# Kernel optimization log

Hardware: AMD Instinct MI355X
Metric: run time of the kernel (lower is better)

The kernel has to match this reference:

```python
import math
import jax, jax.numpy as jnp
import numpy as np

SR = 44100
N_HARMONICS = 64
EPS = 1e-5
LOG10 = math.log(10.0)


def scale_function(x):
    # ddsp_pytorch util.scale_function: 2 * sigmoid(x)**log(10) + 1e-7
    return 2.0 * jax.nn.sigmoid(x) ** LOG10 + 1e-7


def setup_inputs() -> dict:
    key = jax.random.key(0)
    k1, k2, k3 = jax.random.split(key, 3)
    bs, n_samples = 32, 64000
    # f0 in [80, 480] Hz so upper harmonics cross Nyquist for some frames
    f0_hz = jax.random.uniform(k1, (bs, n_samples), dtype=jnp.float32) * 400.0 + 80.0
    harmonic_amplitudes = jax.random.normal(k2, (bs, n_samples, N_HARMONICS + 1), dtype=jnp.float32)
    phase = jax.random.uniform(k3, (bs,), dtype=jnp.float32) * 2.0 * jnp.pi
    return {"f0_hz": f0_hz, "harmonic_amplitudes": harmonic_amplitudes, "phase": phase}


def reference(f0_hz, harmonic_amplitudes, phase):
    ha = scale_function(harmonic_amplitudes)            # (bs, S, H+1)
    f0 = f0_hz[..., None]                               # (bs, S, 1)
    total_amplitude = ha[..., :1]                       # (bs, S, 1)
    ha = ha[..., 1:]                                    # (bs, S, H)
    harm = jnp.arange(1, N_HARMONICS + 1, dtype=f0.dtype)  # (H,)
    # anti-alias: zero harmonics above Nyquist
    aa = (f0 * harm < SR / 2).astype(f0.dtype)
    ha_aa = ha * aa
    ha_aa = ha_aa / (jnp.sum(ha_aa, axis=-1, keepdims=True) + EPS)
    ha_aa = ha_aa * total_amplitude
    # phase integration
    omega = jnp.cumsum(2.0 * jnp.pi * f0 / SR, axis=1)  # (bs, S, 1)
    omega = omega + phase.reshape(-1, 1, 1)
    omegas = omega * harm                               # (bs, S, H)
    signal = jnp.sum(jnp.sin(omegas) * ha_aa, axis=-1)  # (bs, S)
    return signal
```

## Files before the change

kernel.cpp:

```cpp
#include <hip/hip_runtime.h>
#include <math.h>

#define BATCH    32
#define CHUNK    128
#define NCHUNK   500
#define TAB_N    1152

__device__ __forceinline__ float scale_fn(float x) {
    float e = exp2f(-1.4426950408889634f * x);
    float l = log2f(1.0f + e);
    return 2.0f * exp2f(-2.302585092994046f * l) + 1e-7f;
}

__global__ __launch_bounds__(128) void table_kernel(float* __restrict__ gtab) {
    int i = blockIdx.x * 128 + threadIdx.x;
    if (i < TAB_N) gtab[i] = scale_fn(fmaf((float)i, 0.015625f, -8.0f));
}

__global__ __launch_bounds__(128) void chunk_sum_kernel(
        const float* __restrict__ f0, double* __restrict__ csum) {
    int bx = blockIdx.x;
    int t  = threadIdx.x;
    double v = (double)f0[(long)bx * CHUNK + t];
    for (int off = 32; off > 0; off >>= 1) v += __shfl_down(v, off, 64);
    __shared__ double ws[2];
    if ((t & 63) == 0) ws[t >> 6] = v;
    __syncthreads();
    if (t == 0) csum[bx] = ws[0] + ws[1];
}

__global__ __launch_bounds__(512) void chunk_scan_kernel(double* __restrict__ csum) {
    int r = blockIdx.x;
    int t = threadIdx.x;
    int lane = t & 63, w = t >> 6;
    double orig = (t < NCHUNK) ? csum[(long)r * NCHUNK + t] : 0.0;
    double v = orig;
    for (int off = 1; off < 64; off <<= 1) {
        double n = __shfl_up(v, off, 64);
        if (lane >= off) v += n;
    }
    __shared__ double wsum[8];
    if (lane == 63) wsum[w] = v;
    __syncthreads();
    double add = 0.0;
    for (int i = 0; i < w; ++i) add += wsum[i];
    v += add;
    if (t < NCHUNK) csum[(long)r * NCHUNK + t] = v - orig;
}

__global__ __launch_bounds__(128) void osc_kernel(
        const float* __restrict__ f0,
        const float* __restrict__ ha,
        const float* __restrict__ phase,
        const double* __restrict__ csum,
        const float* __restrict__ gtab,
        float* __restrict__ out) {
    int bx = blockIdx.x;
    int r  = bx / NCHUNK;
    int t  = threadIdx.x;
    int lane = t & 63, w = t >> 6;

    long sbase = (long)bx * CHUNK;
    const float* hablk = ha + sbase * 65;

    __shared__ float amp[CHUNK * 65];
    __shared__ float tab[TAB_N];

    {
        const float4* ts = (const float4*)gtab;
        float4* td = (float4*)tab;
        td[t]       = ts[t];
        td[t + 128] = ts[t + 128];
        if (t < 32) td[t + 256] = ts[t + 256];
    }
    {
        const float4* src = (const float4*)hablk;
        float4* dst = (float4*)amp;
        #pragma unroll
        for (int i = 0; i < 16; ++i)
            dst[i * 128 + t] = src[i * 128 + t];
        if (t < 32)
            dst[16 * 128 + t] = src[16 * 128 + t];
    }

    float f0v = f0[sbase + t];

    double v = (double)f0v;
    for (int off = 1; off < 64; off <<= 1) {
        double n = __shfl_up(v, off, 64);
        if (lane >= off) v += n;
    }
    __shared__ double wsum[2];
    if (lane == 63) wsum[w] = v;
    __syncthreads();
    if (w == 1) v += wsum[0];
    v += csum[bx];
    double x = v * (1.0 / 44100.0) + (double)phase[r] * 0.15915494309189535;
    x -= floor(x);
    float nu = (float)x;

    float k0 = floorf(22050.0f / f0v);
    if (f0v * (k0 + 1.0f) < 22050.0f)      k0 += 1.0f;
    else if (!(f0v * k0 < 22050.0f))       k0 -= 1.0f;

    float th = 6.283185307179586f * nu;
    float s1 = __sinf(th);
    float c1 = __cosf(th);
    float s = s1, c = c1;

    float S1 = 0.0f, S2 = 0.0f;
    #pragma unroll 8
    for (int h = 0; h < 64; ++h) {
        float a  = amp[t * 65 + 1 + h];
        float tc = fmaf(a, 64.0f, 512.0f);
        tc = fminf(fmaxf(tc, 0.0f), 1022.99f);
        float fi = floorf(tc);
        int   i  = (int)fi;
        float fr = tc - fi;
        float w0 = tab[i];
        float w1 = tab[i + 1];
        float wv = fmaf(fr, w1 - w0, w0);
        wv = ((float)(h + 1) <= k0) ? wv : 0.0f;
        S1 += wv;
        S2 = fmaf(wv, s, S2);
        float ns = fmaf(s, c1,  c * s1);
        float nc = fmaf(c, c1, -(s * s1));
        s = ns; c = nc;
    }

    float total = scale_fn(amp[t * 65]);
    out[sbase + t] = total * S2 / (S1 + 1e-5f);
}

extern "C" void kernel_launch(void* const* d_in, const int* in_sizes, int n_in,
                              void* d_out, int out_size, void* d_ws, size_t ws_size,
                              hipStream_t stream) {
    const float* f0    = (const float*)d_in[0];
    const float* ha    = (const float*)d_in[1];
    const float* phase = (const float*)d_in[2];
    float* out = (float*)d_out;

    double* csum = (double*)d_ws;
    float*  gtab = (float*)((char*)d_ws + 131072);

    table_kernel<<<(TAB_N + 127) / 128, 128, 0, stream>>>(gtab);
    chunk_sum_kernel<<<BATCH * NCHUNK, CHUNK, 0, stream>>>(f0, csum);
    chunk_scan_kernel<<<BATCH, 512, 0, stream>>>(csum);
    osc_kernel<<<BATCH * NCHUNK, CHUNK, 0, stream>>>(f0, ha, phase, csum, gtab, out);
}
```

Measured before the change: 703.0 us.

## Compute scaled amplitudes during load into fp16 LDS slab, drop lookup table

Replaces the precomputed lookup-table interpolation with a direct sigmoid-power evaluation done while loading from global memory. Results are stored as fp16 in a padded shared slab, with the anti-alias mask applied at that point. The inner loop then reads half2 pairs and uses a two-term Chebyshev sine recurrence. This cuts shared memory (allowing the occupancy hint of 4) and removes the per-harmonic table gathers. In exchange the transcendental work moves into the load phase, and fp16 storage (scaled by 256) costs some precision.

```diff
diff --git a/kernel.cpp b/kernel.cpp
--- a/kernel.cpp
+++ b/kernel.cpp
@@ -1,20 +1,16 @@
 #include <hip/hip_runtime.h>
+#include <hip/hip_fp16.h>
 #include <math.h>
 
-#define BATCH    32
-#define CHUNK    128
-#define NCHUNK   500
-#define TAB_N    1152
+#define BATCH      32
+#define CHUNK      128
+#define NCHUNK     500
+#define SLABSTRIDE 66
 
-__device__ __forceinline__ float scale_fn(float x) {
+__device__ __forceinline__ float scale256(float x) {
     float e = exp2f(-1.4426950408889634f * x);
     float l = log2f(1.0f + e);
-    return 2.0f * exp2f(-2.302585092994046f * l) + 1e-7f;
-}
-
-__global__ __launch_bounds__(128) void table_kernel(float* __restrict__ gtab) {
-    int i = blockIdx.x * 128 + threadIdx.x;
-    if (i < TAB_N) gtab[i] = scale_fn(fmaf((float)i, 0.015625f, -8.0f));
+    return fmaf(512.0f, exp2f(-2.302585092994046f * l), 256.0f * 1e-7f);
 }
 
 __global__ __launch_bounds__(128) void chunk_sum_kernel(
@@ -48,12 +44,30 @@
     if (t < NCHUNK) csum[(long)r * NCHUNK + t] = v - orig;
 }
 
-__global__ __launch_bounds__(128) void osc_kernel(
+__device__ __forceinline__ void process4(float4 v, int e,
+        __half* __restrict__ slab, float* __restrict__ amp0,
+        const float* __restrict__ f0s) {
+    int s = e / 65;
+    int c = e - s * 65;
+    float vals[4] = {v.x, v.y, v.z, v.w};
+    #pragma unroll
+    for (int k = 0; k < 4; ++k) {
+        float wv = scale256(vals[k]);
+        if (c == 0) {
+            amp0[s] = wv * 0.00390625f;
+        } else {
+            bool keep = f0s[s] * (float)c < 22050.0f;
+            slab[s * SLABSTRIDE + (c - 1)] = __float2half(keep ? wv : 0.0f);
+        }
+        if (++c == 65) { c = 0; ++s; }
+    }
+}
+
+__global__ __launch_bounds__(128, 4) void osc_kernel(
         const float* __restrict__ f0,
         const float* __restrict__ ha,
         const float* __restrict__ phase,
         const double* __restrict__ csum,
-        const float* __restrict__ gtab,
         float* __restrict__ out) {
     int bx = blockIdx.x;
     int r  = bx / NCHUNK;
@@ -61,36 +75,32 @@
     int lane = t & 63, w = t >> 6;
 
     long sbase = (long)bx * CHUNK;
-    const float* hablk = ha + sbase * 65;
 
-    __shared__ float amp[CHUNK * 65];
-    __shared__ float tab[TAB_N];
+    __shared__ __half slab[CHUNK * SLABSTRIDE];
+    __shared__ float  amp0[CHUNK];
+    __shared__ float  f0s[CHUNK];
+    __shared__ double wsum[2];
 
-    {
-        const float4* ts = (const float4*)gtab;
-        float4* td = (float4*)tab;
-        td[t]       = ts[t];
-        td[t + 128] = ts[t + 128];
-        if (t < 32) td[t + 256] = ts[t + 256];
+    if (t < 32) ((float4*)f0s)[t] = ((const float4*)(f0 + sbase))[t];
+    __syncthreads();
+
+    const float4* src = (const float4*)(ha + sbase * 65);
+    #pragma unroll 4
+    for (int i = 0; i < 16; ++i) {
+        float4 v = src[i * 128 + t];
+        process4(v, (i * 128 + t) * 4, slab, amp0, f0s);
     }
-    {
-        const float4* src = (const float4*)hablk;
-        float4* dst = (float4*)amp;
-        #pragma unroll
-        for (int i = 0; i < 16; ++i)
-            dst[i * 128 + t] = src[i * 128 + t];
-        if (t < 32)
-            dst[16 * 128 + t] = src[16 * 128 + t];
+    if (t < 32) {
+        float4 v = src[2048 + t];
+        process4(v, (2048 + t) * 4, slab, amp0, f0s);
     }
 
-    float f0v = f0[sbase + t];
-
+    float f0v = f0s[t];
     double v = (double)f0v;
     for (int off = 1; off < 64; off <<= 1) {
         double n = __shfl_up(v, off, 64);
         if (lane >= off) v += n;
     }
-    __shared__ double wsum[2];
     if (lane == 63) wsum[w] = v;
     __syncthreads();
     if (w == 1) v += wsum[0];
@@ -99,52 +109,38 @@
     x -= floor(x);
     float nu = (float)x;
 
-    float k0 = floorf(22050.0f / f0v);
-    if (f0v * (k0 + 1.0f) < 22050.0f)      k0 += 1.0f;
-    else if (!(f0v * k0 < 22050.0f))       k0 -= 1.0f;
-
     float th = 6.283185307179586f * nu;
-    float s1 = __sinf(th);
-    float c1 = __cosf(th);
-    float s = s1, c = c1;
+    float sA = __sinf(th);
+    float c2 = 2.0f * __cosf(th);
+    float sB = c2 * sA;
 
     float S1 = 0.0f, S2 = 0.0f;
-    #pragma unroll 8
-    for (int h = 0; h < 64; ++h) {
-        float a  = amp[t * 65 + 1 + h];
-        float tc = fmaf(a, 64.0f, 512.0f);
-        tc = fminf(fmaxf(tc, 0.0f), 1022.99f);
-        float fi = floorf(tc);
-        int   i  = (int)fi;
-        float fr = tc - fi;
-        float w0 = tab[i];
-        float w1 = tab[i + 1];
-        float wv = fmaf(fr, w1 - w0, w0);
-        wv = ((float)(h + 1) <= k0) ? wv : 0.0f;
-        S1 += wv;
-        S2 = fmaf(wv, s, S2);
-        float ns = fmaf(s, c1,  c * s1);
-        float nc = fmaf(c, c1, -(s * s1));
-        s = ns; c = nc;
+    const __half2* row = (const __half2*)(slab + t * SLABSTRIDE);
+    #pragma unroll
+    for (int j = 0; j < 32; ++j) {
+        float2 w2 = __half22float2(row[j]);
+        S1 += w2.x; S2 = fmaf(w2.x, sA, S2);
+        S1 += w2.y; S2 = fmaf(w2.y, sB, S2);
+        float sn1 = fmaf(c2, sB, -sA);
+        float sn2 = fmaf(c2, sn1, -sB);
+        sA = sn1; sB = sn2;
     }
 
-    float total = scale_fn(amp[t * 65]);
-    out[sbase + t] = total * S2 / (S1 + 1e-5f);
+    out[sbase + t] = amp0[t] * S2 / (S1 + 256.0f * 1e-5f);
 }
 
 extern "C" void kernel_launch(void* const* d_in, const int* in_sizes, int n_in,
                               void* d_out, int out_size, void* d_ws, size_t ws_size,
                               hipStream_t stream) {
+    (void)in_sizes; (void)n_in; (void)out_size; (void)ws_size;
     const float* f0    = (const float*)d_in[0];
     const float* ha    = (const float*)d_in[1];
     const float* phase = (const float*)d_in[2];
     float* out = (float*)d_out;
 
     double* csum = (double*)d_ws;
-    float*  gtab = (float*)((char*)d_ws + 131072);
 
-    table_kernel<<<(TAB_N + 127) / 128, 128, 0, stream>>>(gtab);
     chunk_sum_kernel<<<BATCH * NCHUNK, CHUNK, 0, stream>>>(f0, csum);
     chunk_scan_kernel<<<BATCH, 512, 0, stream>>>(csum);
-    osc_kernel<<<BATCH * NCHUNK, CHUNK, 0, stream>>>(f0, ha, phase, csum, gtab, out);
+    osc_kernel<<<BATCH * NCHUNK, CHUNK, 0, stream>>>(f0, ha, phase, csum, out);
 }
```

After: 749.8 us. +6.7%, slower.

## Split harmonics across four lanes per sample with 512-thread oscillator blocks

Applied to the files above, without the earlier changes.

The oscillator kernel now launches 512 threads per 128-sample chunk, and each sample's 64 harmonics are divided among 4 lanes of 16 harmonics each. Partial sums are combined with cross-lane shuffles. The harmonic sine recurrence is replaced by a Chebyshev two-term recurrence seeded per lane from directly computed sines, and the phase scan runs on only the first 128 threads via shared memory. The aim is more threads in flight to hide global and LDS latency, and shorter serial dependency chains per thread, at the cost of extra barriers and shuffles and fewer resident blocks per CU given the shared-memory footprint.

```diff
diff --git a/kernel.cpp b/kernel.cpp
--- a/kernel.cpp
+++ b/kernel.cpp
@@ -48,7 +48,7 @@
     if (t < NCHUNK) csum[(long)r * NCHUNK + t] = v - orig;
 }
 
-__global__ __launch_bounds__(128) void osc_kernel(
+__global__ __launch_bounds__(512, 4) void osc_kernel(
         const float* __restrict__ f0,
         const float* __restrict__ ha,
         const float* __restrict__ phase,
@@ -63,78 +63,106 @@
     long sbase = (long)bx * CHUNK;
     const float* hablk = ha + sbase * 65;
 
-    __shared__ float amp[CHUNK * 65];
-    __shared__ float tab[TAB_N];
+    __shared__ float  amp[CHUNK * 65];
+    __shared__ float  tab[TAB_N];
+    __shared__ float  f0s[CHUNK];
+    __shared__ float  nuA[CHUNK];
+    __shared__ double wsum[2];
 
-    {
-        const float4* ts = (const float4*)gtab;
-        float4* td = (float4*)tab;
-        td[t]       = ts[t];
-        td[t + 128] = ts[t + 128];
-        if (t < 32) td[t + 256] = ts[t + 256];
-    }
+    if (t < 288) ((float4*)tab)[t] = ((const float4*)gtab)[t];
+    if (t < 32)  ((float4*)f0s)[t] = ((const float4*)(f0 + sbase))[t];
     {
         const float4* src = (const float4*)hablk;
         float4* dst = (float4*)amp;
         #pragma unroll
-        for (int i = 0; i < 16; ++i)
-            dst[i * 128 + t] = src[i * 128 + t];
-        if (t < 32)
-            dst[16 * 128 + t] = src[16 * 128 + t];
+        for (int i = 0; i < 4; ++i)
+            dst[i * 512 + t] = src[i * 512 + t];
+        if (t < 32) dst[2048 + t] = src[2048 + t];
     }
+    __syncthreads();
 
-    float f0v = f0[sbase + t];
+    double v = 0.0;
+    if (t < 128) {
+        v = (double)f0s[t];
+        for (int off = 1; off < 64; off <<= 1) {
+            double n = __shfl_up(v, off, 64);
+            if (lane >= off) v += n;
+        }
+        if (lane == 63) wsum[w] = v;
+    }
+    __syncthreads();
+    if (t < 128) {
+        if (w == 1) v += wsum[0];
+        v += csum[bx];
+        double x = v * (1.0 / 44100.0) + (double)phase[r] * 0.15915494309189535;
+        x -= floor(x);
+        nuA[t] = (float)x;
+    }
+    __syncthreads();
 
-    double v = (double)f0v;
-    for (int off = 1; off < 64; off <<= 1) {
-        double n = __shfl_up(v, off, 64);
-        if (lane >= off) v += n;
-    }
-    __shared__ double wsum[2];
-    if (lane == 63) wsum[w] = v;
-    __syncthreads();
-    if (w == 1) v += wsum[0];
-    v += csum[bx];
-    double x = v * (1.0 / 44100.0) + (double)phase[r] * 0.15915494309189535;
-    x -= floor(x);
-    float nu = (float)x;
+    int s  = w * 16 + (lane & 15);
+    int q  = lane >> 4;
+    int h0 = q * 16;
+
+    float f0v = f0s[s];
+    float nu  = nuA[s];
 
     float k0 = floorf(22050.0f / f0v);
     if (f0v * (k0 + 1.0f) < 22050.0f)      k0 += 1.0f;
     else if (!(f0v * k0 < 22050.0f))       k0 -= 1.0f;
 
-    float th = 6.283185307179586f * nu;
-    float s1 = __sinf(th);
-    float c1 = __cosf(th);
-    float s = s1, c = c1;
+    float c2;
+    {
+        float th = 6.283185307179586f * nu;
+        c2 = 2.0f * __cosf(th);
+    }
+    float m1 = (float)(h0 + 1) * nu; m1 -= floorf(m1);
+    float m2 = (float)(h0 + 2) * nu; m2 -= floorf(m2);
+    float sA = __sinf(6.283185307179586f * m1);
+    float sB = 6.283185307179586f * m2;  sB = __sinf(sB);
+
+    const float* arow = amp + s * 65 + 1 + h0;
 
     float S1 = 0.0f, S2 = 0.0f;
-    #pragma unroll 8
-    for (int h = 0; h < 64; ++h) {
-        float a  = amp[t * 65 + 1 + h];
-        float tc = fmaf(a, 64.0f, 512.0f);
-        tc = fminf(fmaxf(tc, 0.0f), 1022.99f);
-        float fi = floorf(tc);
-        int   i  = (int)fi;
-        float fr = tc - fi;
-        float w0 = tab[i];
-        float w1 = tab[i + 1];
-        float wv = fmaf(fr, w1 - w0, w0);
-        wv = ((float)(h + 1) <= k0) ? wv : 0.0f;
-        S1 += wv;
-        S2 = fmaf(wv, s, S2);
-        float ns = fmaf(s, c1,  c * s1);
-        float nc = fmaf(c, c1, -(s * s1));
-        s = ns; c = nc;
+    #pragma unroll
+    for (int j = 0; j < 16; j += 2) {
+        float a0 = arow[j];
+        float a1 = arow[j + 1];
+        float tc0 = fmaf(a0, 64.0f, 512.0f);
+        tc0 = fminf(fmaxf(tc0, 0.0f), 1022.99f);
+        float fi0 = floorf(tc0); int i0 = (int)fi0; float fr0 = tc0 - fi0;
+        float w0 = fmaf(fr0, tab[i0 + 1] - tab[i0], tab[i0]);
+        float tc1 = fmaf(a1, 64.0f, 512.0f);
+        tc1 = fminf(fmaxf(tc1, 0.0f), 1022.99f);
+        float fi1 = floorf(tc1); int i1 = (int)fi1; float fr1 = tc1 - fi1;
+        float w1 = fmaf(fr1, tab[i1 + 1] - tab[i1], tab[i1]);
+
+        w0 = ((float)(h0 + 1 + j) <= k0) ? w0 : 0.0f;
+        w1 = ((float)(h0 + 2 + j) <= k0) ? w1 : 0.0f;
+
+        S1 += w0; S2 = fmaf(w0, sA, S2);
+        S1 += w1; S2 = fmaf(w1, sB, S2);
+
+        float sn1 = fmaf(c2, sB, -sA);
+        float sn2 = fmaf(c2, sn1, -sB);
+        sA = sn1; sB = sn2;
     }
 
-    float total = scale_fn(amp[t * 65]);
-    out[sbase + t] = total * S2 / (S1 + 1e-5f);
+    S1 += __shfl_xor(S1, 16, 64);
+    S1 += __shfl_xor(S1, 32, 64);
+    S2 += __shfl_xor(S2, 16, 64);
+    S2 += __shfl_xor(S2, 32, 64);
+
+    if (q == 0) {
+        float total = scale_fn(amp[s * 65]);
+        out[sbase + s] = total * S2 / (S1 + 1e-5f);
+    }
 }
 
 extern "C" void kernel_launch(void* const* d_in, const int* in_sizes, int n_in,
                               void* d_out, int out_size, void* d_ws, size_t ws_size,
                               hipStream_t stream) {
+    (void)in_sizes; (void)n_in; (void)out_size; (void)ws_size;
     const float* f0    = (const float*)d_in[0];
     const float* ha    = (const float*)d_in[1];
     const float* phase = (const float*)d_in[2];
@@ -146,5 +174,5 @@
     table_kernel<<<(TAB_N + 127) / 128, 128, 0, stream>>>(gtab);
     chunk_sum_kernel<<<BATCH * NCHUNK, CHUNK, 0, stream>>>(f0, csum);
     chunk_scan_kernel<<<BATCH, 512, 0, stream>>>(csum);
-    osc_kernel<<<BATCH * NCHUNK, CHUNK, 0, stream>>>(f0, ha, phase, csum, gtab, out);
+    osc_kernel<<<BATCH * NCHUNK, 512, 0, stream>>>(f0, ha, phase, csum, gtab, out);
 }
```

Measured after the change: 692.4 us. No clear change (-1.5%).
